# Kernel tuning notes

Measured on AMD Instinct MI355X. Metric: run time of the kernel, lower is better.

The kernel has to match this reference:

```python
import jax, jax.numpy as jnp
import numpy as np

DG, K, PAD = 4, 3, 1  # deformable_groups, kernel_size, padding=(K-1)//2
K2 = K * K


def setup_inputs() -> dict:
    key = jax.random.key(0)
    k1, k2, k3, k4 = jax.random.split(key, 4)
    B, C, H, W, O = 2, 256, 200, 200, 256
    x = jax.random.normal(k1, (B, C, H, W), jnp.float32)
    # conv_offset_mask params (zero-init in the module; small random here so the
    # deformable gather is actually exercised with nonzero offsets/masks)
    w_om = jax.random.normal(k2, (DG * 3 * K2, C, K, K), jnp.float32) * 0.01
    b_om = jax.random.normal(k3, (DG * 3 * K2,), jnp.float32) * 0.1
    # ModulatedDeformConv weight (bias=False)
    w_dcn = jax.random.normal(k4, (O, C, K, K), jnp.float32) * (1.0 / np.sqrt(C * K2))
    return {"x": x, "w_om": w_om, "b_om": b_om, "w_dcn": w_dcn}


def _mdcn(x, offset, mask, weight):
    """Modulated deformable conv v2, stride 1, padding PAD, no bias.
    offset: [B, DG*2*K2, H, W] interpreted (per DCNv2 CUDA kernel) as
            [B, DG, K2, 2(dy,dx), H, W]; mask: [B, DG*K2, H, W]."""
    B, C, H, W = x.shape
    Cg = C // DG
    off = offset.reshape(B, DG, K2, 2, H, W)
    dy, dx = off[:, :, :, 0], off[:, :, :, 1]          # [B,DG,K2,H,W]
    m = mask.reshape(B, DG, K2, H, W)
    ki = jnp.repeat(jnp.arange(K), K)                  # kernel row per tap
    kj = jnp.tile(jnp.arange(K), K)                    # kernel col per tap
    hh = jnp.arange(H, dtype=x.dtype)
    ww = jnp.arange(W, dtype=x.dtype)
    # absolute sampling positions [B,DG,K2,H,W]
    py = hh[None, None, None, :, None] - PAD + ki[None, None, :, None, None] + dy
    px = ww[None, None, None, None, :] - PAD + kj[None, None, :, None, None] + dx
    y0 = jnp.floor(py)
    x0 = jnp.floor(px)
    wy = py - y0
    wx = px - x0
    y0i = y0.astype(jnp.int32)
    x0i = x0.astype(jnp.int32)
    xf = x.reshape(B, DG, Cg, H * W)

    def gather(yi, xi):
        valid = ((yi >= 0) & (yi < H) & (xi >= 0) & (xi < W)).astype(x.dtype)
        idx = jnp.clip(yi, 0, H - 1) * W + jnp.clip(xi, 0, W - 1)
        g = jnp.take_along_axis(xf, idx.reshape(B, DG, 1, K2 * H * W), axis=3)
        return g.reshape(B, DG, Cg, K2, H, W) * valid[:, :, None]

    # bilinear sample with zero padding outside, [B,DG,Cg,K2,H,W]
    v = (gather(y0i, x0i) * ((1 - wy) * (1 - wx))[:, :, None]
         + gather(y0i, x0i + 1) * ((1 - wy) * wx)[:, :, None]
         + gather(y0i + 1, x0i) * (wy * (1 - wx))[:, :, None]
         + gather(y0i + 1, x0i + 1) * (wy * wx)[:, :, None])
    v = v * m[:, :, None]
    wr = weight.reshape(-1, DG, Cg, K2)  # [O,DG,Cg,K2]
    return jnp.einsum('ogck,bgckhw->bohw', wr, v)


def reference(x, w_om, b_om, w_dcn):
    om = jax.lax.conv_general_dilated(
        x, w_om, (1, 1), ((PAD, PAD), (PAD, PAD)),
        dimension_numbers=('NCHW', 'OIHW', 'NCHW')) + b_om[None, :, None, None]
    o1, o2, mask = jnp.split(om, 3, axis=1)
    offset = jnp.concatenate([o1, o2], axis=1)
    mask = jax.nn.sigmoid(mask)
    return jax.nn.relu(_mdcn(x, offset, mask, w_dcn))
```

## Files before the change

kernel.cpp:

```cpp
#include <hip/hip_runtime.h>
#include <math.h>

#define HH 200
#define WW 200
#define CIN 256
#define OMCH 108
#define OCH 256
#define NPIX (HH*WW)

typedef _Float16 f16x8 __attribute__((ext_vector_type(8)));
typedef float floatx4 __attribute__((ext_vector_type(4)));

static __device__ __forceinline__ unsigned short f16bits(float v) {
    _Float16 h = (_Float16)v;
    return __builtin_bit_cast(unsigned short, h);
}
static __device__ __forceinline__ _Float16 f16lo(unsigned int u) {
    return __builtin_bit_cast(_Float16, (unsigned short)(u & 0xffffu));
}
static __device__ __forceinline__ _Float16 f16hi(unsigned int u) {
    return __builtin_bit_cast(_Float16, (unsigned short)(u >> 16));
}

static __device__ __forceinline__ int xcd_swizzle(int orig, int nwg) {
    int q = nwg >> 3, r = nwg & 7;
    int x = orig & 7, rank = orig >> 3;
    int base = (x < r) ? x * (q + 1) : r * (q + 1) + (x - r) * q;
    return base + rank;
}

__global__ __launch_bounds__(256) void transpose_x(const float* __restrict__ x,
                                                   unsigned short* __restrict__ xT) {
    __shared__ __align__(16) unsigned short st[64][264];
    int t = threadIdx.x;
    int blk = blockIdx.x;
    int b = blk / 625, pix0 = (blk % 625) * 64;
    const float* xb = x + (size_t)b * CIN * NPIX + pix0;
    int p = t & 63, oct = t >> 6;

    for (int c32 = 0; c32 < CIN; c32 += 32) {
        int c = c32 + oct * 8;
        union { unsigned short u[8]; float4 f; } pk;
#pragma unroll
        for (int i = 0; i < 8; i++)
            pk.u[i] = f16bits(xb[(size_t)(c + i) * NPIX + p]);
        *(float4*)&st[p][c] = pk.f;
    }
    __syncthreads();
    int p2 = t >> 2, qo = t & 3;
    unsigned short* dst = xT + ((size_t)b * NPIX + pix0 + p2) * CIN + qo * 64;
#pragma unroll
    for (int j = 0; j < 8; j++)
        *(float4*)(dst + j * 8) = *(const float4*)&st[p2][qo * 64 + j * 8];
}

__global__ void prep_wom(const float* __restrict__ w, unsigned short* __restrict__ wom3) {
    int i = blockIdx.x * 256 + threadIdx.x;
    int slice = i >> 12, rem = i & 4095;
    int oc = rem >> 5, qj = rem & 31;
    int ks = slice & 1, it = slice >> 1;
    int tap = it >> 2, c64 = it & 3;
    int c = c64 * 64 + ks * 32 + qj;
    float v = (oc < OMCH) ? w[(size_t)oc * 2304 + c * 9 + tap] : 0.f;
    wom3[i] = f16bits(v);
}

__global__ void prep_wdcn(const float* __restrict__ w, unsigned short* __restrict__ wt3) {
    int i = blockIdx.x * 256 + threadIdx.x;
    int slice = i >> 13, rem = i & 8191;
    int oc = rem >> 5, qj = rem & 31;
    int ks = slice & 1, gk = slice >> 1;
    int g = gk / 9, kk = gk % 9;
    int cin = g * 64 + ks * 32 + qj;
    wt3[i] = f16bits(w[(size_t)oc * 2304 + cin * 9 + kk]);
}

__global__ __launch_bounds__(512, 6) void om_mfma(const unsigned short* __restrict__ xT,
                                                  const unsigned short* __restrict__ wom3,
                                                  const float* __restrict__ bom,
                                                  float* __restrict__ om) {
    __shared__ __align__(16) unsigned short vtile[3][114][72];

    int t = threadIdx.x;
    int lane = t & 63, n16 = t & 15, quad = (lane >> 4) & 3, wv = t >> 6;
    int ocbase = (wv & 3) * 32;
    int wh = wv >> 2;

    int bid = xcd_swizzle(blockIdx.x, 800);
    int b = bid / 400, rem0 = bid - b * 400;
    int h = rem0 >> 1, hf = rem0 & 1;
    int c0 = hf * 100;
    const unsigned short* xtb = xT + (size_t)b * NPIX * CIN;

    floatx4 acc[2][4];
#pragma unroll
    for (int i = 0; i < 2; i++)
#pragma unroll
        for (int j = 0; j < 4; j++) acc[i][j] = (floatx4){0.f, 0.f, 0.f, 0.f};

    for (int chunk = 0; chunk < 4; chunk++) {
        if (chunk) __syncthreads();

        for (int k = 0; k < 6; k++) {
            int L = t + k * 512;
            if (L < 2736) {
                int r3 = L / 912, r2 = L - r3 * 912;
                int cc = r2 >> 3, u16 = r2 & 7;
                int gr = h - 1 + r3, gc = c0 - 1 + cc;
                float4 v = {0.f, 0.f, 0.f, 0.f};
                if ((unsigned)gr < (unsigned)HH && (unsigned)gc < (unsigned)WW && cc < 102)
                    v = *(const float4*)(xtb + (size_t)(gr * WW + gc) * CIN + chunk * 64 + u16 * 8);
                *(float4*)&vtile[r3][cc][u16 * 8] = v;
            }
        }
        __syncthreads();

#pragma unroll 3
        for (int tap = 0; tap < 9; tap++) {
            int r3 = tap / 3, dj = tap - r3 * 3;
            int colb = dj + wh * 64 + n16;
#pragma unroll
            for (int ks = 0; ks < 2; ks++) {
                int ch = ks * 32 + quad * 8;
                f16x8 bf0 = *(const f16x8*)&vtile[r3][colb     ][ch];
                f16x8 bf1 = *(const f16x8*)&vtile[r3][colb + 16][ch];
                f16x8 bf2 = *(const f16x8*)&vtile[r3][colb + 32][ch];
                const unsigned short* wb = wom3 + (size_t)((tap * 4 + chunk) * 2 + ks) * 4096
                                           + (ocbase + n16) * 32 + quad * 8;
                f16x8 a0 = *(const f16x8*)wb;
                f16x8 a1 = *(const f16x8*)(wb + 512);
                acc[0][0] = __builtin_amdgcn_mfma_f32_16x16x32_f16(a0, bf0, acc[0][0], 0, 0, 0);
                acc[1][0] = __builtin_amdgcn_mfma_f32_16x16x32_f16(a1, bf0, acc[1][0], 0, 0, 0);
                acc[0][1] = __builtin_amdgcn_mfma_f32_16x16x32_f16(a0, bf1, acc[0][1], 0, 0, 0);
                acc[1][1] = __builtin_amdgcn_mfma_f32_16x16x32_f16(a1, bf1, acc[1][1], 0, 0, 0);
                acc[0][2] = __builtin_amdgcn_mfma_f32_16x16x32_f16(a0, bf2, acc[0][2], 0, 0, 0);
                acc[1][2] = __builtin_amdgcn_mfma_f32_16x16x32_f16(a1, bf2, acc[1][2], 0, 0, 0);
                if (wh == 0) {
                    f16x8 bf3 = *(const f16x8*)&vtile[r3][colb + 48][ch];
                    acc[0][3] = __builtin_amdgcn_mfma_f32_16x16x32_f16(a0, bf3, acc[0][3], 0, 0, 0);
                    acc[1][3] = __builtin_amdgcn_mfma_f32_16x16x32_f16(a1, bf3, acc[1][3], 0, 0, 0);
                }
            }
        }
    }

    int hbase = h * WW + c0;
#pragma unroll
    for (int oi = 0; oi < 2; oi++) {
        int oc0 = ocbase + oi * 16 + quad * 4;
        if (oc0 < OMCH) {
#pragma unroll
            for (int tile = 0; tile < 4; tile++) {
                if (wh && tile == 3) continue;
                int pl = (wh * 4 + tile) * 16 + n16;
                if (pl < 100) {
#pragma unroll
                    for (int r = 0; r < 4; r++) {
                        int oc = oc0 + r;
                        if (oc < OMCH)
                            om[((size_t)(b * OMCH + oc)) * NPIX + hbase + pl]
                                = acc[oi][tile][r] + bom[oc];
                    }
                }
            }
        }
    }
}

__global__ __launch_bounds__(512, 6) void dcn_mfma(const unsigned short* __restrict__ xT,
                                                   const float* __restrict__ om,
                                                   const unsigned short* __restrict__ wt3,
                                                   float* __restrict__ out) {
    __shared__ unsigned int iPk[36 * 64];
    __shared__ uint2        wPk[36 * 64];
    __shared__ __align__(16) unsigned short vbuf[2][64][72];

    int t = threadIdx.x;
    int l = t & 63;
    int oct = t >> 6;
    int p8 = l >> 3;
    int chunk = l & 7;
    int mypix = oct * 8 + p8;
    int n16 = t & 15, quad = l >> 4;
    int ocbase = oct * 32;

    int gp0 = xcd_swizzle(blockIdx.x, 1250) * 64;
    int b = gp0 / NPIX;
    int pix0 = gp0 - b * NPIX;
    const unsigned short* xtb = xT + (size_t)b * NPIX * CIN;
    const float* omb = om + (size_t)b * OMCH * NPIX;

    for (int r = t; r < 36 * 64; r += 512) {
        int gk = r >> 6, p = r & 63;
        int g = gk / 9, kk = gk % 9;
        int ki = kk / 3, kj = kk % 3;
        int pp = pix0 + p;
        int hh = pp / WW, ww2 = pp % WW;
        float dy = omb[(size_t)(g * 18 + 2 * kk    ) * NPIX + pp];
        float dx = omb[(size_t)(g * 18 + 2 * kk + 1) * NPIX + pp];
        float mr = omb[(size_t)(72 + g * 9 + kk    ) * NPIX + pp];
        float m = 1.f / (1.f + __expf(-mr));
        float py = (float)(hh - 1 + ki) + dy;
        float px = (float)(ww2 - 1 + kj) + dx;
        float fy = floorf(py), fx = floorf(px);
        float wy = py - fy, wx = px - fx;
        int y0 = (int)fy, x0 = (int)fx, y1 = y0 + 1, x1 = x0 + 1;
        bool vy0 = (y0 >= 0) && (y0 < HH), vy1 = (y1 >= 0) && (y1 < HH);
        bool vx0 = (x0 >= 0) && (x0 < WW), vx1 = (x1 >= 0) && (x1 < WW);
        int cy0 = min(max(y0, 0), HH - 1), cy1 = min(max(y1, 0), HH - 1);
        int cx0 = min(max(x0, 0), WW - 1), cx1 = min(max(x1, 0), WW - 1);
        float w00 = (vy0 && vx0) ? (1.f - wy) * (1.f - wx) * m : 0.f;
        float w01 = (vy0 && vx1) ? (1.f - wy) * wx * m : 0.f;
        float w10 = (vy1 && vx0) ? wy * (1.f - wx) * m : 0.f;
        float w11 = (vy1 && vx1) ? wy * wx * m : 0.f;
        int i00 = cy0 * WW + cx0;
        unsigned int dx1 = (unsigned int)(cx1 - cx0);
        unsigned int dy1 = (unsigned int)(cy1 - cy0);
        iPk[r] = (unsigned int)i00 | (dx1 << 16) | (dy1 << 17);
        uint2 wp;
        wp.x = (unsigned int)f16bits(w00) | ((unsigned int)f16bits(w01) << 16);
        wp.y = (unsigned int)f16bits(w10) | ((unsigned int)f16bits(w11) << 16);
        wPk[r] = wp;
    }
    __syncthreads();

    floatx4 acc[2][4];
#pragma unroll
    for (int i = 0; i < 2; i++)
#pragma unroll
        for (int j = 0; j < 4; j++) acc[i][j] = (floatx4){0.f, 0.f, 0.f, 0.f};

    unsigned int ipNext; uint2 wpNext;

    {
        unsigned int ip = iPk[mypix];
        uint2 wp = wPk[mypix];
        int i00 = ip & 0xffff;
        int dx1 = (ip >> 16) & 1, dy1 = (ip >> 17) & 1;
        int i01 = i00 + dx1, i10 = i00 + dy1 * WW, i11 = i10 + dx1;
        const unsigned short* xg = xtb + chunk * 8;
        f16x8 c00 = *(const f16x8*)(xg + (size_t)i00 * CIN);
        f16x8 c01 = *(const f16x8*)(xg + (size_t)i01 * CIN);
        f16x8 c10 = *(const f16x8*)(xg + (size_t)i10 * CIN);
        f16x8 c11 = *(const f16x8*)(xg + (size_t)i11 * CIN);
        ipNext = iPk[64 + mypix];
        wpNext = wPk[64 + mypix];
        f16x8 v = c00 * f16lo(wp.x) + c01 * f16hi(wp.x)
                + c10 * f16lo(wp.y) + c11 * f16hi(wp.y);
        *(float4*)&vbuf[0][mypix][chunk * 8] = __builtin_bit_cast(float4, v);
    }
    __syncthreads();

    for (int gk = 0; gk < 36; gk++) {
        int cur = gk & 1;
        bool have = (gk < 35);

        _Float16 nw00, nw01, nw10, nw11;
        f16x8 n00, n01, n10, n11;
        if (have) {
            unsigned int ip = ipNext; uint2 wp = wpNext;
            int i00 = ip & 0xffff;
            int dx1 = (ip >> 16) & 1, dy1 = (ip >> 17) & 1;
            int i01 = i00 + dx1, i10 = i00 + dy1 * WW, i11 = i10 + dx1;
            const unsigned short* xg = xtb + ((gk + 1) / 9) * 64 + chunk * 8;
            n00 = *(const f16x8*)(xg + (size_t)i00 * CIN);
            n01 = *(const f16x8*)(xg + (size_t)i01 * CIN);
            n10 = *(const f16x8*)(xg + (size_t)i10 * CIN);
            n11 = *(const f16x8*)(xg + (size_t)i11 * CIN);
            nw00 = f16lo(wp.x); nw01 = f16hi(wp.x);
            nw10 = f16lo(wp.y); nw11 = f16hi(wp.y);
        }
        if (gk < 34) {
            ipNext = iPk[(gk + 2) * 64 + mypix];
            wpNext = wPk[(gk + 2) * 64 + mypix];
        }

#pragma unroll
        for (int ks = 0; ks < 2; ks++) {
            f16x8 bf0 = *(const f16x8*)&vbuf[cur][n16     ][ks * 32 + quad * 8];
            f16x8 bf1 = *(const f16x8*)&vbuf[cur][16 + n16][ks * 32 + quad * 8];
            f16x8 bf2 = *(const f16x8*)&vbuf[cur][32 + n16][ks * 32 + quad * 8];
            f16x8 bf3 = *(const f16x8*)&vbuf[cur][48 + n16][ks * 32 + quad * 8];
#pragma unroll
            for (int oi = 0; oi < 2; oi++) {
                f16x8 a = *(const f16x8*)&wt3[(size_t)(gk * 2 + ks) * 8192
                                              + (ocbase + oi * 16 + n16) * 32 + quad * 8];
                acc[oi][0] = __builtin_amdgcn_mfma_f32_16x16x32_f16(a, bf0, acc[oi][0], 0, 0, 0);
                acc[oi][1] = __builtin_amdgcn_mfma_f32_16x16x32_f16(a, bf1, acc[oi][1], 0, 0, 0);
                acc[oi][2] = __builtin_amdgcn_mfma_f32_16x16x32_f16(a, bf2, acc[oi][2], 0, 0, 0);
                acc[oi][3] = __builtin_amdgcn_mfma_f32_16x16x32_f16(a, bf3, acc[oi][3], 0, 0, 0);
            }
        }

        if (have) {
            f16x8 v = n00 * nw00 + n01 * nw01 + n10 * nw10 + n11 * nw11;
            *(float4*)&vbuf[cur ^ 1][mypix][chunk * 8] = __builtin_bit_cast(float4, v);
            __syncthreads();
        }
    }

#pragma unroll
    for (int oi = 0; oi < 2; oi++)
#pragma unroll
        for (int pt = 0; pt < 4; pt++) {
            int gpix = pix0 + pt * 16 + n16;
#pragma unroll
            for (int r = 0; r < 4; r++) {
                int oc = ocbase + oi * 16 + quad * 4 + r;
                out[((size_t)(b * OCH + oc)) * NPIX + gpix] = fmaxf(acc[oi][pt][r], 0.f);
            }
        }
}

extern "C" void kernel_launch(void* const* d_in, const int* in_sizes, int n_in,
                              void* d_out, int out_size, void* d_ws, size_t ws_size,
                              hipStream_t stream) {
    const float* x     = (const float*)d_in[0];
    const float* w_om  = (const float*)d_in[1];
    const float* b_om  = (const float*)d_in[2];
    const float* w_dcn = (const float*)d_in[3];
    float* out = (float*)d_out;

    char* ws = (char*)d_ws;
    float*          om   = (float*)(ws);
    unsigned short* xT   = (unsigned short*)(ws + 34560000);
    unsigned short* wom3 = (unsigned short*)(ws + 75520000);
    unsigned short* wt3  = (unsigned short*)(ws + 76109824);

    transpose_x<<<1250, 256, 0, stream>>>(x, xT);
    prep_wom   <<<1152, 256, 0, stream>>>(w_om, wom3);
    prep_wdcn  <<<2304, 256, 0, stream>>>(w_dcn, wt3);
    om_mfma    <<< 800, 512, 0, stream>>>(xT, wom3, b_om, om);
    dcn_mfma   <<<1250, 512, 0, stream>>>(xT, om, wt3, out);
}
```

Measured before the change: 394.1 us.

## Deepen gather prefetch to two stages in DCN MFMA loop, lower occupancy bound

Restructures the main loop into a 2-step unrolled loop with two register sets for bilinear gather loads, so global loads for step gk+2 and gk+3 are issued two MFMA phases before they are packed into LDS. This hides more gather latency behind MFMA work. The extra live f16x8 registers are accommodated by relaxing launch_bounds min blocks from 6 to 4, trading occupancy for per-wave latency hiding.

```diff
diff --git a/kernel.cpp b/kernel.cpp
--- a/kernel.cpp
+++ b/kernel.cpp
@@ -167,7 +167,7 @@
     }
 }
 
-__global__ __launch_bounds__(512, 6) void dcn_mfma(const unsigned short* __restrict__ xT,
+__global__ __launch_bounds__(512, 4) void dcn_mfma(const unsigned short* __restrict__ xT,
                                                    const float* __restrict__ om,
                                                    const unsigned short* __restrict__ wt3,
                                                    float* __restrict__ out) {
@@ -232,69 +232,74 @@
 
     unsigned int ipNext; uint2 wpNext;
 
-    {
-        unsigned int ip = iPk[mypix];
-        uint2 wp = wPk[mypix];
-        int i00 = ip & 0xffff;
-        int dx1 = (ip >> 16) & 1, dy1 = (ip >> 17) & 1;
-        int i01 = i00 + dx1, i10 = i00 + dy1 * WW, i11 = i10 + dx1;
-        const unsigned short* xg = xtb + chunk * 8;
-        f16x8 c00 = *(const f16x8*)(xg + (size_t)i00 * CIN);
-        f16x8 c01 = *(const f16x8*)(xg + (size_t)i01 * CIN);
-        f16x8 c10 = *(const f16x8*)(xg + (size_t)i10 * CIN);
-        f16x8 c11 = *(const f16x8*)(xg + (size_t)i11 * CIN);
-        ipNext = iPk[64 + mypix];
-        wpNext = wPk[64 + mypix];
-        f16x8 v = c00 * f16lo(wp.x) + c01 * f16hi(wp.x)
-                + c10 * f16lo(wp.y) + c11 * f16hi(wp.y);
-        *(float4*)&vbuf[0][mypix][chunk * 8] = __builtin_bit_cast(float4, v);
-    }
+#define DCN_PRELOAD(GKN)                                                        \
+    do {                                                                        \
+        ipNext = iPk[(GKN) * 64 + mypix];                                       \
+        wpNext = wPk[(GKN) * 64 + mypix];                                       \
+    } while (0)
+
+#define DCN_ISSUE(C00, C01, C10, C11, SWP, GKN)                                 \
+    do {                                                                        \
+        unsigned int ip_ = ipNext; SWP = wpNext;                                \
+        int i00_ = ip_ & 0xffff;                                                \
+        int dx1_ = (ip_ >> 16) & 1, dy1_ = (ip_ >> 17) & 1;                     \
+        int i01_ = i00_ + dx1_, i10_ = i00_ + dy1_ * WW, i11_ = i10_ + dx1_;    \
+        const unsigned short* xg_ = xtb + ((GKN) / 9) * 64 + chunk * 8;         \
+        C00 = *(const f16x8*)(xg_ + (size_t)i00_ * CIN);                        \
+        C01 = *(const f16x8*)(xg_ + (size_t)i01_ * CIN);                        \
+        C10 = *(const f16x8*)(xg_ + (size_t)i10_ * CIN);                        \
+        C11 = *(const f16x8*)(xg_ + (size_t)i11_ * CIN);                        \
+    } while (0)
+
+#define DCN_PACK(C00, C01, C10, C11, SWP, DSTBUF)                               \
+    do {                                                                        \
+        f16x8 v_ = C00 * f16lo(SWP.x) + C01 * f16hi(SWP.x)                      \
+                 + C10 * f16lo(SWP.y) + C11 * f16hi(SWP.y);                     \
+        *(float4*)&vbuf[DSTBUF][mypix][chunk * 8] = __builtin_bit_cast(float4, v_); \
+    } while (0)
+
+#define DCN_MFMA_PHASE(BUF, GKI)                                                \
+    do {                                                                        \
+        _Pragma("unroll")                                                       \
+        for (int ks = 0; ks < 2; ks++) {                                        \
+            f16x8 bf0 = *(const f16x8*)&vbuf[BUF][n16     ][ks * 32 + quad * 8]; \
+            f16x8 bf1 = *(const f16x8*)&vbuf[BUF][16 + n16][ks * 32 + quad * 8]; \
+            f16x8 bf2 = *(const f16x8*)&vbuf[BUF][32 + n16][ks * 32 + quad * 8]; \
+            f16x8 bf3 = *(const f16x8*)&vbuf[BUF][48 + n16][ks * 32 + quad * 8]; \
+            _Pragma("unroll")                                                   \
+            for (int oi = 0; oi < 2; oi++) {                                    \
+                f16x8 a = *(const f16x8*)&wt3[(size_t)((GKI) * 2 + ks) * 8192   \
+                                              + (ocbase + oi * 16 + n16) * 32 + quad * 8]; \
+                acc[oi][0] = __builtin_amdgcn_mfma_f32_16x16x32_f16(a, bf0, acc[oi][0], 0, 0, 0); \
+                acc[oi][1] = __builtin_amdgcn_mfma_f32_16x16x32_f16(a, bf1, acc[oi][1], 0, 0, 0); \
+                acc[oi][2] = __builtin_amdgcn_mfma_f32_16x16x32_f16(a, bf2, acc[oi][2], 0, 0, 0); \
+                acc[oi][3] = __builtin_amdgcn_mfma_f32_16x16x32_f16(a, bf3, acc[oi][3], 0, 0, 0); \
+            }                                                                   \
+        }                                                                       \
+    } while (0)
+
+    f16x8 a00, a01, a10, a11, b00, b01, b10, b11;
+    uint2 wpA, wpB;
+    DCN_PRELOAD(0);
+    DCN_ISSUE(a00, a01, a10, a11, wpA, 0);
+    DCN_PRELOAD(1);
+    DCN_ISSUE(b00, b01, b10, b11, wpB, 1);
+    DCN_PRELOAD(2);
+    DCN_PACK(a00, a01, a10, a11, wpA, 0);
     __syncthreads();
 
-    for (int gk = 0; gk < 36; gk++) {
-        int cur = gk & 1;
-        bool have = (gk < 35);
-
-        _Float16 nw00, nw01, nw10, nw11;
-        f16x8 n00, n01, n10, n11;
-        if (have) {
-            unsigned int ip = ipNext; uint2 wp = wpNext;
-            int i00 = ip & 0xffff;
-            int dx1 = (ip >> 16) & 1, dy1 = (ip >> 17) & 1;
-            int i01 = i00 + dx1, i10 = i00 + dy1 * WW, i11 = i10 + dx1;
-            const unsigned short* xg = xtb + ((gk + 1) / 9) * 64 + chunk * 8;
-            n00 = *(const f16x8*)(xg + (size_t)i00 * CIN);
-            n01 = *(const f16x8*)(xg + (size_t)i01 * CIN);
-            n10 = *(const f16x8*)(xg + (size_t)i10 * CIN);
-            n11 = *(const f16x8*)(xg + (size_t)i11 * CIN);
-            nw00 = f16lo(wp.x); nw01 = f16hi(wp.x);
-            nw10 = f16lo(wp.y); nw11 = f16hi(wp.y);
-        }
-        if (gk < 34) {
-            ipNext = iPk[(gk + 2) * 64 + mypix];
-            wpNext = wPk[(gk + 2) * 64 + mypix];
-        }
-
-#pragma unroll
-        for (int ks = 0; ks < 2; ks++) {
-            f16x8 bf0 = *(const f16x8*)&vbuf[cur][n16     ][ks * 32 + quad * 8];
-            f16x8 bf1 = *(const f16x8*)&vbuf[cur][16 + n16][ks * 32 + quad * 8];
-            f16x8 bf2 = *(const f16x8*)&vbuf[cur][32 + n16][ks * 32 + quad * 8];
-            f16x8 bf3 = *(const f16x8*)&vbuf[cur][48 + n16][ks * 32 + quad * 8];
-#pragma unroll
-            for (int oi = 0; oi < 2; oi++) {
-                f16x8 a = *(const f16x8*)&wt3[(size_t)(gk * 2 + ks) * 8192
-                                              + (ocbase + oi * 16 + n16) * 32 + quad * 8];
-                acc[oi][0] = __builtin_amdgcn_mfma_f32_16x16x32_f16(a, bf0, acc[oi][0], 0, 0, 0);
-                acc[oi][1] = __builtin_amdgcn_mfma_f32_16x16x32_f16(a, bf1, acc[oi][1], 0, 0, 0);
-                acc[oi][2] = __builtin_amdgcn_mfma_f32_16x16x32_f16(a, bf2, acc[oi][2], 0, 0, 0);
-                acc[oi][3] = __builtin_amdgcn_mfma_f32_16x16x32_f16(a, bf3, acc[oi][3], 0, 0, 0);
-            }
-        }
-
-        if (have) {
-            f16x8 v = n00 * nw00 + n01 * nw01 + n10 * nw10 + n11 * nw11;
-            *(float4*)&vbuf[cur ^ 1][mypix][chunk * 8] = __builtin_bit_cast(float4, v);
+#pragma unroll 1
+    for (int gk = 0; gk < 36; gk += 2) {
+        if (gk + 2 < 36) DCN_ISSUE(a00, a01, a10, a11, wpA, gk + 2);
+        if (gk + 3 < 36) DCN_PRELOAD(gk + 3);
+        DCN_MFMA_PHASE(0, gk);
+        DCN_PACK(b00, b01, b10, b11, wpB, 1);
+        __syncthreads();
+        if (gk + 3 < 36) DCN_ISSUE(b00, b01, b10, b11, wpB, gk + 3);
+        if (gk + 4 < 36) DCN_PRELOAD(gk + 4);
+        DCN_MFMA_PHASE(1, gk + 1);
+        if (gk + 2 < 36) {
+            DCN_PACK(a00, a01, a10, a11, wpA, 0);
             __syncthreads();
         }
     }
@@ -310,6 +315,10 @@
                 out[((size_t)(b * OCH + oc)) * NPIX + gpix] = fmaxf(acc[oi][pt][r], 0.f);
             }
         }
+#undef DCN_PRELOAD
+#undef DCN_ISSUE
+#undef DCN_PACK
+#undef DCN_MFMA_PHASE
 }
 
 extern "C" void kernel_launch(void* const* d_in, const int* in_sizes, int n_in,
```

After: 458.4 us. +16.3%, slower.
